# Optimization experiments

Measured on AMD Instinct MI355X. Metric: run time of the kernel, lower is better.

## Reference

```python
import jax, jax.numpy as jnp
import numpy as np

N = 50000      # num_nodes
E = 1600000    # num edges (avg degree 32)
C_IN = 32      # in_channels / out_channels
HID = 128      # hidden_dim
LAT = 64       # latent_dim


def setup_inputs() -> dict:
    key = jax.random.key(0)
    ks = jax.random.split(key, 16)
    f32 = jnp.float32
    def w(k, shape, fan_in):
        return (jax.random.uniform(k, shape, dtype=f32) * 2.0 - 1.0) / np.sqrt(fan_in)
    return {
        "x": jax.random.normal(ks[0], (N, C_IN), dtype=f32),
        "edge_index": jax.random.randint(ks[1], (2, E), 0, N, dtype=jnp.int32),
        "eps": jax.random.normal(ks[2], (LAT,), dtype=f32),
        # GCNConv1
        "W1": w(ks[3], (C_IN, HID), C_IN), "b1": jnp.zeros((HID,), f32),
        # GCNConv2
        "W2": w(ks[4], (HID, HID), HID), "b2": jnp.zeros((HID,), f32),
        # fc_mu / fc_logvar
        "Wmu": w(ks[5], (HID, LAT), HID), "bmu": jnp.zeros((LAT,), f32),
        "Wlv": w(ks[6], (HID, LAT), HID), "blv": jnp.zeros((LAT,), f32),
        # decoder fc1 / fc2
        "Wd1": w(ks[7], (LAT, HID), LAT), "bd1": jnp.zeros((HID,), f32),
        "Wd2": w(ks[8], (HID, N * C_IN), HID), "bd2": jnp.zeros((N * C_IN,), f32),
    }


def _gcn_norm(edge_index):
    # Add self-loops, compute symmetric normalization D^-1/2 (A+I) D^-1/2 (PyG GCNConv default).
    loop = jnp.arange(N, dtype=edge_index.dtype)
    src = jnp.concatenate([edge_index[0], loop])
    dst = jnp.concatenate([edge_index[1], loop])
    deg = jax.ops.segment_sum(jnp.ones_like(dst, dtype=jnp.float32), dst, num_segments=N)
    dis = jnp.where(deg > 0, jax.lax.rsqrt(jnp.maximum(deg, 1.0)), 0.0)
    norm = dis[src] * dis[dst]  # [E+N]
    return src, dst, norm


def _gcn(x, W, b, src, dst, norm):
    h = x @ W                           # transform first: [N, out]
    m = h[src] * norm[:, None]          # gather + scale  (irregular)
    agg = jax.ops.segment_sum(m, dst, num_segments=N)  # scatter-add
    return agg + b


def reference(x, edge_index, eps, W1, b1, W2, b2, Wmu, bmu, Wlv, blv, Wd1, bd1, Wd2, bd2):
    src, dst, norm = _gcn_norm(edge_index)
    h = jax.nn.relu(_gcn(x, W1, b1, src, dst, norm))
    h = jax.nn.relu(_gcn(h, W2, b2, src, dst, norm))
    g = h.mean(axis=0)                  # [HID]
    mu = g @ Wmu + bmu                  # [LAT]
    logvar = g @ Wlv + blv              # [LAT]
    z = mu + eps * jnp.exp(0.5 * logvar)
    d = jax.nn.relu(z @ Wd1 + bd1)      # [HID]
    recon = (d @ Wd2 + bd2).reshape(N, C_IN)
    return recon, mu, logvar
```

## Files before the change

kernel.cpp:

```cpp
#include <hip/hip_runtime.h>
#include <math.h>

#define NN 50000
#define EE 1600000
#define CIN 32
#define HIDDEN 128
#define LATENT 64
#define NM 1600000

#define OFF_CNT     0u
#define OFF_CURSOR  204800u
#define OFF_ROWPTR  409600u
#define OFF_DIS     614400u
#define OFF_CSRSRC  819200u
#define OFF_CSRNRM  7219200u
#define OFF_HA      13619200u
#define OFF_HB      39219200u
#define OFF_GSUM    64819200u
#define OFF_DVEC    64819712u

__global__ void k_count(const int* __restrict__ dst, int* __restrict__ cnt) {
    int e = blockIdx.x * 256 + threadIdx.x;
    if (e < EE) atomicAdd(&cnt[dst[e]], 1);
}

__global__ void k_dis(const int* __restrict__ cnt, float* __restrict__ dis) {
    int i = blockIdx.x * 256 + threadIdx.x;
    if (i < NN) dis[i] = rsqrtf((float)(cnt[i] + 1));
}

__global__ void k_scan(const int* __restrict__ cnt, int* __restrict__ rowptr) {
    __shared__ int sdata[1024];
    __shared__ int running;
    int t = threadIdx.x;
    if (t == 0) running = 0;
    __syncthreads();
    for (int base = 0; base < NN; base += 1024) {
        int i = base + t;
        int v = (i < NN) ? cnt[i] : 0;
        sdata[t] = v;
        __syncthreads();
        for (int off = 1; off < 1024; off <<= 1) {
            int add = (t >= off) ? sdata[t - off] : 0;
            __syncthreads();
            sdata[t] += add;
            __syncthreads();
        }
        if (i < NN) rowptr[i] = running + sdata[t] - v;
        int tot = sdata[1023];
        __syncthreads();
        if (t == 0) running += tot;
        __syncthreads();
    }
    if (t == 0) rowptr[NN] = running;
}

__global__ void k_fill(const int* __restrict__ src, const int* __restrict__ dst,
                       const float* __restrict__ dis, const int* __restrict__ rowptr,
                       int* __restrict__ cursor, int* __restrict__ csr_src,
                       float* __restrict__ csr_nrm) {
    int e = blockIdx.x * 256 + threadIdx.x;
    if (e >= EE) return;
    int d = dst[e], s = src[e];
    int pos = atomicAdd(&cursor[d], 1);
    int slot = rowptr[d] + pos;
    csr_src[slot] = s;
    csr_nrm[slot] = dis[s] * dis[d];
}

__global__ void k_gemm1(const float* __restrict__ x, const float* __restrict__ W1,
                        float* __restrict__ hA) {
    __shared__ float xs[8 * 32];
    int t = threadIdx.x;
    int nb = blockIdx.x * 8;
    xs[t] = x[nb * 32 + t];
    __syncthreads();
    int c = t & 127, quad = t >> 7;
    float a0 = 0.f, a1 = 0.f, a2 = 0.f, a3 = 0.f;
    const float* r0 = &xs[(quad * 4 + 0) * 32];
    const float* r1 = &xs[(quad * 4 + 1) * 32];
    const float* r2 = &xs[(quad * 4 + 2) * 32];
    const float* r3 = &xs[(quad * 4 + 3) * 32];
#pragma unroll
    for (int k = 0; k < 32; k++) {
        float w = W1[k * 128 + c];
        a0 = fmaf(r0[k], w, a0);
        a1 = fmaf(r1[k], w, a1);
        a2 = fmaf(r2[k], w, a2);
        a3 = fmaf(r3[k], w, a3);
    }
    int n0 = nb + quad * 4;
    hA[(n0 + 0) * 128 + c] = a0;
    hA[(n0 + 1) * 128 + c] = a1;
    hA[(n0 + 2) * 128 + c] = a2;
    hA[(n0 + 3) * 128 + c] = a3;
}

__global__ void k_gemm2(const float* __restrict__ hB, const float* __restrict__ W2,
                        float* __restrict__ hA) {
    __shared__ float rs[8 * 128];
    int t = threadIdx.x;
    int nb = blockIdx.x * 8;
#pragma unroll
    for (int r = 0; r < 4; r++) rs[t + r * 256] = hB[nb * 128 + t + r * 256];
    __syncthreads();
    int c = t & 127, quad = t >> 7;
    float a0 = 0.f, a1 = 0.f, a2 = 0.f, a3 = 0.f;
    const float* r0 = &rs[(quad * 4 + 0) * 128];
    const float* r1 = &rs[(quad * 4 + 1) * 128];
    const float* r2 = &rs[(quad * 4 + 2) * 128];
    const float* r3 = &rs[(quad * 4 + 3) * 128];
#pragma unroll 8
    for (int k = 0; k < 128; k++) {
        float w = W2[k * 128 + c];
        a0 = fmaf(r0[k], w, a0);
        a1 = fmaf(r1[k], w, a1);
        a2 = fmaf(r2[k], w, a2);
        a3 = fmaf(r3[k], w, a3);
    }
    int n0 = nb + quad * 4;
    hA[(n0 + 0) * 128 + c] = a0;
    hA[(n0 + 1) * 128 + c] = a1;
    hA[(n0 + 2) * 128 + c] = a2;
    hA[(n0 + 3) * 128 + c] = a3;
}

__global__ void k_agg1(const float* __restrict__ h, const float* __restrict__ dis,
                       const int* __restrict__ rowptr, const int* __restrict__ csr_src,
                       const float* __restrict__ csr_nrm, const float* __restrict__ bias,
                       float* __restrict__ outp) {
    int t = threadIdx.x;
    int c4 = t & 31;
    int i = blockIdx.x * 8 + (t >> 5);
    if (i >= NN) return;
    const float4* h4 = (const float4*)h;
    float di = dis[i];
    float sn = di * di;
    float4 acc = h4[i * 32 + c4];
    acc.x *= sn; acc.y *= sn; acc.z *= sn; acc.w *= sn;
    int beg = rowptr[i], end = rowptr[i + 1];
    for (int s = beg; s < end; s++) {
        int sc = csr_src[s];
        float w = csr_nrm[s];
        float4 hv = h4[sc * 32 + c4];
        acc.x = fmaf(hv.x, w, acc.x);
        acc.y = fmaf(hv.y, w, acc.y);
        acc.z = fmaf(hv.z, w, acc.z);
        acc.w = fmaf(hv.w, w, acc.w);
    }
    float4 bv = ((const float4*)bias)[c4];
    acc.x = fmaxf(acc.x + bv.x, 0.f);
    acc.y = fmaxf(acc.y + bv.y, 0.f);
    acc.z = fmaxf(acc.z + bv.z, 0.f);
    acc.w = fmaxf(acc.w + bv.w, 0.f);
    ((float4*)outp)[i * 32 + c4] = acc;
}

__global__ void k_agg2(const float* __restrict__ h, const float* __restrict__ dis,
                       const int* __restrict__ rowptr, const int* __restrict__ csr_src,
                       const float* __restrict__ csr_nrm, const float* __restrict__ bias,
                       float* __restrict__ gsum) {
    int t = threadIdx.x;
    int c4 = t & 31;
    int slot8 = t >> 5;
    const float4* h4 = (const float4*)h;
    float4 bv = ((const float4*)bias)[c4];
    float4 sum; sum.x = sum.y = sum.z = sum.w = 0.f;
    for (int i = blockIdx.x * 8 + slot8; i < NN; i += gridDim.x * 8) {
        float di = dis[i];
        float sn = di * di;
        float4 acc = h4[i * 32 + c4];
        acc.x *= sn; acc.y *= sn; acc.z *= sn; acc.w *= sn;
        int beg = rowptr[i], end = rowptr[i + 1];
        for (int s = beg; s < end; s++) {
            int sc = csr_src[s];
            float w = csr_nrm[s];
            float4 hv = h4[sc * 32 + c4];
            acc.x = fmaf(hv.x, w, acc.x);
            acc.y = fmaf(hv.y, w, acc.y);
            acc.z = fmaf(hv.z, w, acc.z);
            acc.w = fmaf(hv.w, w, acc.w);
        }
        sum.x += fmaxf(acc.x + bv.x, 0.f);
        sum.y += fmaxf(acc.y + bv.y, 0.f);
        sum.z += fmaxf(acc.z + bv.z, 0.f);
        sum.w += fmaxf(acc.w + bv.w, 0.f);
    }
    __shared__ float4 sdata[256];
    sdata[t] = sum;
    __syncthreads();
    if (t < 32) {
        float4 tot = sdata[t];
#pragma unroll
        for (int s = 1; s < 8; s++) {
            float4 v = sdata[t + s * 32];
            tot.x += v.x; tot.y += v.y; tot.z += v.z; tot.w += v.w;
        }
        atomicAdd(&gsum[c4 * 4 + 0], tot.x);
        atomicAdd(&gsum[c4 * 4 + 1], tot.y);
        atomicAdd(&gsum[c4 * 4 + 2], tot.z);
        atomicAdd(&gsum[c4 * 4 + 3], tot.w);
    }
}

__global__ void k_head(const float* __restrict__ gsum, const float* __restrict__ eps,
                       const float* __restrict__ Wmu, const float* __restrict__ bmu,
                       const float* __restrict__ Wlv, const float* __restrict__ blv,
                       const float* __restrict__ Wd1, const float* __restrict__ bd1,
                       float* __restrict__ outp, float* __restrict__ dvec) {
    __shared__ float g[128];
    __shared__ float zs[64];
    int t = threadIdx.x;
    g[t] = gsum[t] * (1.0f / (float)NN);
    __syncthreads();
    if (t < 64) {
        float mu = bmu[t], lv = blv[t];
#pragma unroll 8
        for (int k = 0; k < 128; k++) {
            float gk = g[k];
            mu = fmaf(gk, Wmu[k * 64 + t], mu);
            lv = fmaf(gk, Wlv[k * 64 + t], lv);
        }
        float z = mu + eps[t] * expf(0.5f * lv);
        outp[NM + t] = mu;
        outp[NM + 64 + t] = lv;
        zs[t] = z;
    }
    __syncthreads();
    float dv = bd1[t];
#pragma unroll 8
    for (int k = 0; k < 64; k++) dv = fmaf(zs[k], Wd1[k * 128 + t], dv);
    dvec[t] = fmaxf(dv, 0.f);
}

__global__ void k_dec(const float* __restrict__ dvec, const float* __restrict__ Wd2,
                      const float* __restrict__ bd2, float* __restrict__ outp) {
    __shared__ float d[128];
    int t = threadIdx.x;
    if (t < 128) d[t] = dvec[t];
    __syncthreads();
    int n0 = (blockIdx.x * 256 + t) * 4;
    if (n0 >= NM) return;
    float4 acc = *(const float4*)(bd2 + n0);
#pragma unroll 8
    for (int k = 0; k < 128; k++) {
        float dk = d[k];
        float4 w = *(const float4*)(Wd2 + (size_t)k * NM + n0);
        acc.x = fmaf(dk, w.x, acc.x);
        acc.y = fmaf(dk, w.y, acc.y);
        acc.z = fmaf(dk, w.z, acc.z);
        acc.w = fmaf(dk, w.w, acc.w);
    }
    *(float4*)(outp + n0) = acc;
}

extern "C" void kernel_launch(void* const* d_in, const int* in_sizes, int n_in,
                              void* d_out, int out_size, void* d_ws, size_t ws_size,
                              hipStream_t stream) {
    const float* x   = (const float*)d_in[0];
    const int*   ei  = (const int*)d_in[1];
    const float* eps = (const float*)d_in[2];
    const float* W1  = (const float*)d_in[3];
    const float* b1  = (const float*)d_in[4];
    const float* W2  = (const float*)d_in[5];
    const float* b2  = (const float*)d_in[6];
    const float* Wmu = (const float*)d_in[7];
    const float* bmu = (const float*)d_in[8];
    const float* Wlv = (const float*)d_in[9];
    const float* blv = (const float*)d_in[10];
    const float* Wd1 = (const float*)d_in[11];
    const float* bd1 = (const float*)d_in[12];
    const float* Wd2 = (const float*)d_in[13];
    const float* bd2 = (const float*)d_in[14];
    float* outp = (float*)d_out;
    char* ws = (char*)d_ws;

    int*   cnt     = (int*)(ws + OFF_CNT);
    int*   cursor  = (int*)(ws + OFF_CURSOR);
    int*   rowptr  = (int*)(ws + OFF_ROWPTR);
    float* dis     = (float*)(ws + OFF_DIS);
    int*   csr_src = (int*)(ws + OFF_CSRSRC);
    float* csr_nrm = (float*)(ws + OFF_CSRNRM);
    float* hA      = (float*)(ws + OFF_HA);
    float* hB      = (float*)(ws + OFF_HB);
    float* gsum    = (float*)(ws + OFF_GSUM);
    float* dvec    = (float*)(ws + OFF_DVEC);

    const int* srcp = ei;
    const int* dstp = ei + EE;

    hipMemsetAsync(cnt, 0, NN * sizeof(int), stream);
    hipMemsetAsync(cursor, 0, NN * sizeof(int), stream);
    hipMemsetAsync(gsum, 0, 128 * sizeof(float), stream);

    k_count<<<EE / 256, 256, 0, stream>>>(dstp, cnt);
    k_dis<<<(NN + 255) / 256, 256, 0, stream>>>(cnt, dis);
    k_scan<<<1, 1024, 0, stream>>>(cnt, rowptr);
    k_fill<<<EE / 256, 256, 0, stream>>>(srcp, dstp, dis, rowptr, cursor, csr_src, csr_nrm);

    k_gemm1<<<NN / 8, 256, 0, stream>>>(x, W1, hA);
    k_agg1<<<NN / 8, 256, 0, stream>>>(hA, dis, rowptr, csr_src, csr_nrm, b1, hB);
    k_gemm2<<<NN / 8, 256, 0, stream>>>(hB, W2, hA);
    k_agg2<<<512, 256, 0, stream>>>(hA, dis, rowptr, csr_src, csr_nrm, b2, gsum);
    k_head<<<1, 128, 0, stream>>>(gsum, eps, Wmu, bmu, Wlv, blv, Wd1, bd1, outp, dvec);
    k_dec<<<(NM / 4 + 255) / 256, 256, 0, stream>>>(dvec, Wd2, bd2, outp);
}
```

Before: 1.783 ms.

## Aggregate before transform, store hidden activations in bf16, parallelize CSR scan

```diff
diff --git a/kernel.cpp b/kernel.cpp
--- a/kernel.cpp
+++ b/kernel.cpp
@@ -12,12 +12,20 @@
 #define OFF_CURSOR  204800u
 #define OFF_ROWPTR  409600u
 #define OFF_DIS     614400u
-#define OFF_CSRSRC  819200u
-#define OFF_CSRNRM  7219200u
-#define OFF_HA      13619200u
-#define OFF_HB      39219200u
-#define OFF_GSUM    64819200u
-#define OFF_DVEC    64819712u
+#define OFF_BSUM    819200u
+#define OFF_CSRSRC  820224u
+#define OFF_CSRNRM  7220224u
+#define OFF_XA      13620224u
+#define OFF_Q       20020224u
+#define OFF_QA      32820224u
+#define OFF_GSUM    58420224u
+#define OFF_DVEC    58420736u
+
+static __device__ __forceinline__ unsigned short f2bf_rne(float f) {
+    unsigned int u = __float_as_uint(f);
+    u += 0x7FFFu + ((u >> 16) & 1u);
+    return (unsigned short)(u >> 16);
+}
 
 __global__ void k_count(const int* __restrict__ dst, int* __restrict__ cnt) {
     int e = blockIdx.x * 256 + threadIdx.x;
@@ -29,30 +37,43 @@
     if (i < NN) dis[i] = rsqrtf((float)(cnt[i] + 1));
 }
 
-__global__ void k_scan(const int* __restrict__ cnt, int* __restrict__ rowptr) {
-    __shared__ int sdata[1024];
-    __shared__ int running;
-    int t = threadIdx.x;
-    if (t == 0) running = 0;
-    __syncthreads();
-    for (int base = 0; base < NN; base += 1024) {
-        int i = base + t;
-        int v = (i < NN) ? cnt[i] : 0;
-        sdata[t] = v;
-        __syncthreads();
-        for (int off = 1; off < 1024; off <<= 1) {
-            int add = (t >= off) ? sdata[t - off] : 0;
-            __syncthreads();
-            sdata[t] += add;
-            __syncthreads();
-        }
-        if (i < NN) rowptr[i] = running + sdata[t] - v;
-        int tot = sdata[1023];
-        __syncthreads();
-        if (t == 0) running += tot;
-        __syncthreads();
-    }
-    if (t == 0) rowptr[NN] = running;
+__global__ void k_scan_local(const int* __restrict__ cnt, int* __restrict__ rowptr,
+                             int* __restrict__ bsum) {
+    __shared__ int s[256];
+    int t = threadIdx.x;
+    int i = blockIdx.x * 256 + t;
+    int v = (i < NN) ? cnt[i] : 0;
+    s[t] = v;
+    __syncthreads();
+    for (int off = 1; off < 256; off <<= 1) {
+        int a = (t >= off) ? s[t - off] : 0;
+        __syncthreads();
+        s[t] += a;
+        __syncthreads();
+    }
+    if (i < NN) rowptr[i] = s[t] - v;
+    if (t == 255) bsum[blockIdx.x] = s[255];
+}
+
+__global__ void k_scan_bsum(int* __restrict__ bsum, int* __restrict__ rowptr, int nblk) {
+    __shared__ int s[256];
+    int t = threadIdx.x;
+    int v = (t < nblk) ? bsum[t] : 0;
+    s[t] = v;
+    __syncthreads();
+    for (int off = 1; off < 256; off <<= 1) {
+        int a = (t >= off) ? s[t - off] : 0;
+        __syncthreads();
+        s[t] += a;
+        __syncthreads();
+    }
+    if (t < nblk) bsum[t] = s[t] - v;
+    if (t == 255) rowptr[NN] = s[255];
+}
+
+__global__ void k_scan_add(int* __restrict__ rowptr, const int* __restrict__ bsum) {
+    int i = blockIdx.x * 256 + threadIdx.x;
+    if (i < NN) rowptr[i] += bsum[blockIdx.x];
 }
 
 __global__ void k_fill(const int* __restrict__ src, const int* __restrict__ dst,
@@ -68,12 +89,37 @@
     csr_nrm[slot] = dis[s] * dis[d];
 }
 
-__global__ void k_gemm1(const float* __restrict__ x, const float* __restrict__ W1,
-                        float* __restrict__ hA) {
+__global__ void k_aggx(const float* __restrict__ x, const float* __restrict__ dis,
+                       const int* __restrict__ rowptr, const int* __restrict__ csr_src,
+                       const float* __restrict__ csr_nrm, float* __restrict__ xa) {
+    int t = threadIdx.x;
+    int c4 = t & 7;
+    int i = blockIdx.x * 32 + (t >> 3);
+    if (i >= NN) return;
+    const float4* x4 = (const float4*)x;
+    float di = dis[i];
+    float sn = di * di;
+    float4 acc = x4[i * 8 + c4];
+    acc.x *= sn; acc.y *= sn; acc.z *= sn; acc.w *= sn;
+    int beg = rowptr[i], end = rowptr[i + 1];
+    for (int s = beg; s < end; s++) {
+        int sc = csr_src[s];
+        float w = csr_nrm[s];
+        float4 v = x4[sc * 8 + c4];
+        acc.x = fmaf(v.x, w, acc.x);
+        acc.y = fmaf(v.y, w, acc.y);
+        acc.z = fmaf(v.z, w, acc.z);
+        acc.w = fmaf(v.w, w, acc.w);
+    }
+    ((float4*)xa)[i * 8 + c4] = acc;
+}
+
+__global__ void k_gemm1h(const float* __restrict__ xa, const float* __restrict__ W1,
+                         const float* __restrict__ b1, unsigned short* __restrict__ q) {
     __shared__ float xs[8 * 32];
     int t = threadIdx.x;
     int nb = blockIdx.x * 8;
-    xs[t] = x[nb * 32 + t];
+    xs[t] = xa[nb * 32 + t];
     __syncthreads();
     int c = t & 127, quad = t >> 7;
     float a0 = 0.f, a1 = 0.f, a2 = 0.f, a3 = 0.f;
@@ -89,118 +135,76 @@
         a2 = fmaf(r2[k], w, a2);
         a3 = fmaf(r3[k], w, a3);
     }
+    float bc = b1[c];
     int n0 = nb + quad * 4;
-    hA[(n0 + 0) * 128 + c] = a0;
-    hA[(n0 + 1) * 128 + c] = a1;
-    hA[(n0 + 2) * 128 + c] = a2;
-    hA[(n0 + 3) * 128 + c] = a3;
-}
-
-__global__ void k_gemm2(const float* __restrict__ hB, const float* __restrict__ W2,
-                        float* __restrict__ hA) {
-    __shared__ float rs[8 * 128];
-    int t = threadIdx.x;
-    int nb = blockIdx.x * 8;
-#pragma unroll
-    for (int r = 0; r < 4; r++) rs[t + r * 256] = hB[nb * 128 + t + r * 256];
-    __syncthreads();
-    int c = t & 127, quad = t >> 7;
-    float a0 = 0.f, a1 = 0.f, a2 = 0.f, a3 = 0.f;
-    const float* r0 = &rs[(quad * 4 + 0) * 128];
-    const float* r1 = &rs[(quad * 4 + 1) * 128];
-    const float* r2 = &rs[(quad * 4 + 2) * 128];
-    const float* r3 = &rs[(quad * 4 + 3) * 128];
-#pragma unroll 8
-    for (int k = 0; k < 128; k++) {
-        float w = W2[k * 128 + c];
-        a0 = fmaf(r0[k], w, a0);
-        a1 = fmaf(r1[k], w, a1);
-        a2 = fmaf(r2[k], w, a2);
-        a3 = fmaf(r3[k], w, a3);
-    }
-    int n0 = nb + quad * 4;
-    hA[(n0 + 0) * 128 + c] = a0;
-    hA[(n0 + 1) * 128 + c] = a1;
-    hA[(n0 + 2) * 128 + c] = a2;
-    hA[(n0 + 3) * 128 + c] = a3;
-}
-
-__global__ void k_agg1(const float* __restrict__ h, const float* __restrict__ dis,
+    q[(n0 + 0) * 128 + c] = f2bf_rne(fmaxf(a0 + bc, 0.f));
+    q[(n0 + 1) * 128 + c] = f2bf_rne(fmaxf(a1 + bc, 0.f));
+    q[(n0 + 2) * 128 + c] = f2bf_rne(fmaxf(a2 + bc, 0.f));
+    q[(n0 + 3) * 128 + c] = f2bf_rne(fmaxf(a3 + bc, 0.f));
+}
+
+__global__ void k_agg2(const unsigned short* __restrict__ q, const float* __restrict__ dis,
                        const int* __restrict__ rowptr, const int* __restrict__ csr_src,
-                       const float* __restrict__ csr_nrm, const float* __restrict__ bias,
-                       float* __restrict__ outp) {
+                       const float* __restrict__ csr_nrm, float* __restrict__ qa) {
     int t = threadIdx.x;
     int c4 = t & 31;
     int i = blockIdx.x * 8 + (t >> 5);
     if (i >= NN) return;
-    const float4* h4 = (const float4*)h;
+    const uint2* q2 = (const uint2*)q;
     float di = dis[i];
     float sn = di * di;
-    float4 acc = h4[i * 32 + c4];
-    acc.x *= sn; acc.y *= sn; acc.z *= sn; acc.w *= sn;
+    uint2 w = q2[i * 32 + c4];
+    float4 acc;
+    acc.x = sn * __uint_as_float(w.x << 16);
+    acc.y = sn * __uint_as_float(w.x & 0xFFFF0000u);
+    acc.z = sn * __uint_as_float(w.y << 16);
+    acc.w = sn * __uint_as_float(w.y & 0xFFFF0000u);
     int beg = rowptr[i], end = rowptr[i + 1];
     for (int s = beg; s < end; s++) {
         int sc = csr_src[s];
-        float w = csr_nrm[s];
-        float4 hv = h4[sc * 32 + c4];
-        acc.x = fmaf(hv.x, w, acc.x);
-        acc.y = fmaf(hv.y, w, acc.y);
-        acc.z = fmaf(hv.z, w, acc.z);
-        acc.w = fmaf(hv.w, w, acc.w);
-    }
-    float4 bv = ((const float4*)bias)[c4];
-    acc.x = fmaxf(acc.x + bv.x, 0.f);
-    acc.y = fmaxf(acc.y + bv.y, 0.f);
-    acc.z = fmaxf(acc.z + bv.z, 0.f);
-    acc.w = fmaxf(acc.w + bv.w, 0.f);
-    ((float4*)outp)[i * 32 + c4] = acc;
-}
-
-__global__ void k_agg2(const float* __restrict__ h, const float* __restrict__ dis,
-                       const int* __restrict__ rowptr, const int* __restrict__ csr_src,
-                       const float* __restrict__ csr_nrm, const float* __restrict__ bias,
-                       float* __restrict__ gsum) {
-    int t = threadIdx.x;
-    int c4 = t & 31;
-    int slot8 = t >> 5;
-    const float4* h4 = (const float4*)h;
-    float4 bv = ((const float4*)bias)[c4];
-    float4 sum; sum.x = sum.y = sum.z = sum.w = 0.f;
-    for (int i = blockIdx.x * 8 + slot8; i < NN; i += gridDim.x * 8) {
-        float di = dis[i];
-        float sn = di * di;
-        float4 acc = h4[i * 32 + c4];
-        acc.x *= sn; acc.y *= sn; acc.z *= sn; acc.w *= sn;
-        int beg = rowptr[i], end = rowptr[i + 1];
-        for (int s = beg; s < end; s++) {
-            int sc = csr_src[s];
-            float w = csr_nrm[s];
-            float4 hv = h4[sc * 32 + c4];
-            acc.x = fmaf(hv.x, w, acc.x);
-            acc.y = fmaf(hv.y, w, acc.y);
-            acc.z = fmaf(hv.z, w, acc.z);
-            acc.w = fmaf(hv.w, w, acc.w);
+        float nw = csr_nrm[s];
+        uint2 v = q2[sc * 32 + c4];
+        acc.x = fmaf(__uint_as_float(v.x << 16), nw, acc.x);
+        acc.y = fmaf(__uint_as_float(v.x & 0xFFFF0000u), nw, acc.y);
+        acc.z = fmaf(__uint_as_float(v.y << 16), nw, acc.z);
+        acc.w = fmaf(__uint_as_float(v.y & 0xFFFF0000u), nw, acc.w);
+    }
+    ((float4*)qa)[i * 32 + c4] = acc;
+}
+
+__global__ void k_gemm2m(const float* __restrict__ qa, const float* __restrict__ W2,
+                         const float* __restrict__ b2, float* __restrict__ gsum) {
+    __shared__ float rs[8 * 128];
+    __shared__ float red[128];
+    int t = threadIdx.x;
+    int c = t & 127, quad = t >> 7;
+    float bc = b2[c];
+    float colsum = 0.f;
+    for (int g = blockIdx.x; g < NN / 8; g += gridDim.x) {
+        int nb = g * 8;
+#pragma unroll
+        for (int r = 0; r < 4; r++) rs[t + r * 256] = qa[nb * 128 + t + r * 256];
+        __syncthreads();
+        float a0 = 0.f, a1 = 0.f, a2 = 0.f, a3 = 0.f;
+        const float* r0 = &rs[(quad * 4 + 0) * 128];
+        const float* r1 = &rs[(quad * 4 + 1) * 128];
+        const float* r2 = &rs[(quad * 4 + 2) * 128];
+        const float* r3 = &rs[(quad * 4 + 3) * 128];
+#pragma unroll 8
+        for (int k = 0; k < 128; k++) {
+            float w = W2[k * 128 + c];
+            a0 = fmaf(r0[k], w, a0);
+            a1 = fmaf(r1[k], w, a1);
+            a2 = fmaf(r2[k], w, a2);
+            a3 = fmaf(r3[k], w, a3);
         }
-        sum.x += fmaxf(acc.x + bv.x, 0.f);
-        sum.y += fmaxf(acc.y + bv.y, 0.f);
-        sum.z += fmaxf(acc.z + bv.z, 0.f);
-        sum.w += fmaxf(acc.w + bv.w, 0.f);
-    }
-    __shared__ float4 sdata[256];
-    sdata[t] = sum;
-    __syncthreads();
-    if (t < 32) {
-        float4 tot = sdata[t];
-#pragma unroll
-        for (int s = 1; s < 8; s++) {
-            float4 v = sdata[t + s * 32];
-            tot.x += v.x; tot.y += v.y; tot.z += v.z; tot.w += v.w;
-        }
-        atomicAdd(&gsum[c4 * 4 + 0], tot.x);
-        atomicAdd(&gsum[c4 * 4 + 1], tot.y);
-        atomicAdd(&gsum[c4 * 4 + 2], tot.z);
-        atomicAdd(&gsum[c4 * 4 + 3], tot.w);
-    }
+        colsum += fmaxf(a0 + bc, 0.f) + fmaxf(a1 + bc, 0.f) +
+                  fmaxf(a2 + bc, 0.f) + fmaxf(a3 + bc, 0.f);
+        __syncthreads();
+    }
+    if (quad == 1) red[c] = colsum;
+    __syncthreads();
+    if (quad == 0) atomicAdd(&gsum[c], colsum + red[c]);
 }
 
 __global__ void k_head(const float* __restrict__ gsum, const float* __restrict__ eps,
@@ -279,29 +283,35 @@
     int*   cursor  = (int*)(ws + OFF_CURSOR);
     int*   rowptr  = (int*)(ws + OFF_ROWPTR);
     float* dis     = (float*)(ws + OFF_DIS);
+    int*   bsum    = (int*)(ws + OFF_BSUM);
     int*   csr_src = (int*)(ws + OFF_CSRSRC);
     float* csr_nrm = (float*)(ws + OFF_CSRNRM);
-    float* hA      = (float*)(ws + OFF_HA);
-    float* hB      = (float*)(ws + OFF_HB);
+    float* xa      = (float*)(ws + OFF_XA);
+    unsigned short* q = (unsigned short*)(ws + OFF_Q);
+    float* qa      = (float*)(ws + OFF_QA);
     float* gsum    = (float*)(ws + OFF_GSUM);
     float* dvec    = (float*)(ws + OFF_DVEC);
 
     const int* srcp = ei;
     const int* dstp = ei + EE;
+
+    const int SCAN_BLKS = (NN + 255) / 256;
 
     hipMemsetAsync(cnt, 0, NN * sizeof(int), stream);
     hipMemsetAsync(cursor, 0, NN * sizeof(int), stream);
     hipMemsetAsync(gsum, 0, 128 * sizeof(float), stream);
 
     k_count<<<EE / 256, 256, 0, stream>>>(dstp, cnt);
-    k_dis<<<(NN + 255) / 256, 256, 0, stream>>>(cnt, dis);
-    k_scan<<<1, 1024, 0, stream>>>(cnt, rowptr);
+    k_dis<<<SCAN_BLKS, 256, 0, stream>>>(cnt, dis);
+    k_scan_local<<<SCAN_BLKS, 256, 0, stream>>>(cnt, rowptr, bsum);
+    k_scan_bsum<<<1, 256, 0, stream>>>(bsum, rowptr, SCAN_BLKS);
+    k_scan_add<<<SCAN_BLKS, 256, 0, stream>>>(rowptr, bsum);
     k_fill<<<EE / 256, 256, 0, stream>>>(srcp, dstp, dis, rowptr, cursor, csr_src, csr_nrm);
 
-    k_gemm1<<<NN / 8, 256, 0, stream>>>(x, W1, hA);
-    k_agg1<<<NN / 8, 256, 0, stream>>>(hA, dis, rowptr, csr_src, csr_nrm, b1, hB);
-    k_gemm2<<<NN / 8, 256, 0, stream>>>(hB, W2, hA);
-    k_agg2<<<512, 256, 0, stream>>>(hA, dis, rowptr, csr_src, csr_nrm, b2, gsum);
+    k_aggx<<<(NN + 31) / 32, 256, 0, stream>>>(x, dis, rowptr, csr_src, csr_nrm, xa);
+    k_gemm1h<<<NN / 8, 256, 0, stream>>>(xa, W1, b1, q);
+    k_agg2<<<NN / 8, 256, 0, stream>>>(q, dis, rowptr, csr_src, csr_nrm, qa);
+    k_gemm2m<<<512, 256, 0, stream>>>(qa, W2, b2, gsum);
     k_head<<<1, 128, 0, stream>>>(gsum, eps, Wmu, bmu, Wlv, blv, Wd1, bd1, outp, dvec);
     k_dec<<<(NM / 4 + 255) / 256, 256, 0, stream>>>(dvec, Wd2, bd2, outp);
 }
```

New measurement: 1.451 ms. 18.6% less time.
